# Optimization experiments

Measured on AMD Instinct MI355X. Metric: run time of the kernel, lower is better.

Reference implementation:

```python
import jax, jax.numpy as jnp
import numpy as np
import math

D = 512
H = 512


def setup_inputs() -> dict:
    key = jax.random.key(0)
    k1, k2, k3, k4 = jax.random.split(key, 4)
    x = jax.random.normal(k1, (32, 2048, D), dtype=jnp.float32)
    h0 = jax.random.normal(k2, (32, H), dtype=jnp.float32)
    Wx = jax.random.normal(k3, (D, 4 * H), dtype=jnp.float32) / math.sqrt(D)
    Wh = jax.random.normal(k4, (H, 4 * H), dtype=jnp.float32) / math.sqrt(H)
    b = jnp.zeros((4 * H,), dtype=jnp.float32)
    return {"x": x, "h0": h0, "Wx": Wx, "Wh": Wh, "b": b}


def lstm_forward(x, h0, Wx, Wh, b):
    # Precompute input projection for all timesteps: (N,T,4H)
    affine_x = jnp.einsum('ntd,dk->ntk', x, Wx) + b
    c0 = jnp.zeros_like(h0)
    Hdim = h0.shape[1]

    def step(carry, ax_t):
        h, c = carry
        affine = ax_t + h @ Wh  # (N,4H)
        i, f, o, g = jnp.split(affine, 4, axis=1)
        i = jax.nn.sigmoid(i)
        f = jax.nn.sigmoid(f)
        o = jax.nn.sigmoid(o)
        g = jnp.tanh(g)
        c_next = f * c + i * g
        h_next = o * jnp.tanh(c_next)
        return (h_next, c_next), h_next

    # scan over time: move T to leading axis
    (_, _), hs = jax.lax.scan(step, (h0, c0), jnp.swapaxes(affine_x, 0, 1))
    return jnp.swapaxes(hs, 0, 1)  # (N,T,H)


def reference(x, h0, Wx, Wh, b):
    return lstm_forward(x, h0, Wx, Wh, b)
```

## Files before the change

kernel.cpp:

```cpp
#include <hip/hip_runtime.h>

typedef __attribute__((ext_vector_type(8))) short short8;
typedef __attribute__((ext_vector_type(8))) unsigned short ushort8;
typedef __attribute__((ext_vector_type(4))) float f32x4;
typedef __attribute__((ext_vector_type(4))) int i32x4;

#define T_STEPS 2048

static __device__ __forceinline__ unsigned short f2bf(float f) {
  unsigned u = __builtin_bit_cast(unsigned, f);
  unsigned r = u + 0x7fffu + ((u >> 16) & 1u);
  return (unsigned short)(r >> 16);
}
static __device__ __forceinline__ float bf2f(unsigned short h) {
  unsigned u = ((unsigned)h) << 16;
  return __builtin_bit_cast(float, u);
}
static __device__ __forceinline__ float fast_sigmoid(float v) {
  return __builtin_amdgcn_rcpf(1.0f + __expf(-v));
}
static __device__ __forceinline__ float fast_tanh(float v) {
  return 1.0f - 2.0f * __builtin_amdgcn_rcpf(1.0f + __expf(2.0f * v));
}

__global__ void prep_kernel(const float* __restrict__ Wx, const float* __restrict__ Wh,
                            const float* __restrict__ h0,
                            unsigned short* __restrict__ wxp, unsigned short* __restrict__ whp,
                            unsigned short* __restrict__ hbuf, int* __restrict__ ctl,
                            int* __restrict__ flags) {
  int idx = blockIdx.x * 256 + threadIdx.x;
  if (idx < 2097152) {
    int which = idx >> 20;
    int r = idx & 1048575;
    int e = r & 7;
    int l = (r >> 3) & 63;
    int kt = (r >> 9) & 15;
    int g = (r >> 13) & 3;
    int s = r >> 15;
    int k = kt * 32 + ((l >> 4) << 3) + e;
    int c = g * 512 + s * 16 + (l & 15);
    const float* W = which ? Wh : Wx;
    unsigned short* dst = which ? whp : wxp;
    dst[r] = f2bf(W[k * 2048 + c]);
  } else if (idx < 2097152 + 16384) {
    int i = idx - 2097152;
    int bg = i >> 9;
    int k = i & 511;
    int g = bg >> 2, bl = bg & 3;
    float v = h0[i];
    unsigned short hi = f2bf(v) & 0xFFFCu;
    unsigned short lo = f2bf(v - bf2f(hi)) & 0xFFFCu;
    unsigned short* d = hbuf + g * 65536;
    d[bl * 512 + k] = hi;
    d[2048 + bl * 512 + k] = lo;
  } else if (idx < 2097152 + 16384 + 9) {
    ctl[idx - (2097152 + 16384)] = 0;
  } else if (idx < 2097152 + 16384 + 9 + 8192) {
    flags[idx - (2097152 + 16384 + 9)] = 0;
  }
}

__global__ void xprep_kernel(const float* __restrict__ x, unsigned short* __restrict__ xb) {
  size_t i8 = ((size_t)blockIdx.x * 256 + threadIdx.x) * 8;
  int t = (int)(i8 >> 14);
  int r = (int)(i8 & 16383);
  int b = r >> 9;
  int d = r & 511;
  const float* src = x + ((size_t)b * 2048 + (size_t)t) * 512 + d;
  f32x4 a = *(const f32x4*)src;
  f32x4 c = *(const f32x4*)(src + 4);
  ushort8 o;
#pragma unroll
  for (int e = 0; e < 4; ++e) {
    o[e] = f2bf(a[e]);
    o[e + 4] = f2bf(c[e]);
  }
  *(ushort8*)(xb + i8) = o;
}

__global__ __launch_bounds__(256, 1) void scan_kernel(
    const unsigned short* __restrict__ xb, const float* __restrict__ bias,
    const unsigned short* __restrict__ wxp, const unsigned short* __restrict__ whp,
    unsigned short* __restrict__ hbuf, float* __restrict__ out, int* __restrict__ ctl,
    int* __restrict__ flags) {
  __shared__ unsigned short WxL[4][16][512];
  __shared__ unsigned short WhL[4][16][512];
  __shared__ float gLDS[2][4][4][4][16];
  __shared__ int s_g, s_s, s_dir;

  const int tid = threadIdx.x;
  const int lane = tid & 63;
  const int gw = tid >> 6;

  if (tid == 0) {
    unsigned xcc;
    asm volatile("s_getreg_b32 %0, hwreg(HW_REG_XCC_ID)" : "=s"(xcc));
    xcc &= 7;
    int tk = __hip_atomic_fetch_add(&ctl[xcc], 1, __ATOMIC_RELAXED,
                                    __HIP_MEMORY_SCOPE_AGENT);
    int c[8];
    for (;;) {
      int tot = 0;
#pragma unroll
      for (int x = 0; x < 8; ++x) {
        c[x] = __hip_atomic_load(&ctl[x], __ATOMIC_RELAXED, __HIP_MEMORY_SCOPE_AGENT);
        tot += c[x];
      }
      if (tot >= 256) break;
      __builtin_amdgcn_s_sleep(2);
    }
    int g = -1, s = -1, dir = 0;
    if (tk < 32) {
      g = (int)xcc;
      s = tk;
      dir = (c[xcc] >= 32);
    } else {
      int rank = __hip_atomic_fetch_add(&ctl[8], 1, __ATOMIC_RELAXED,
                                        __HIP_MEMORY_SCOPE_AGENT);
      int acc2 = 0;
      for (int x = 0; x < 8; ++x) {
        int n = 32 - c[x];
        if (n < 0) n = 0;
        if (g < 0 && rank < acc2 + n) { g = x; s = c[x] + (rank - acc2); }
        acc2 += n;
      }
      dir = 0;
    }
    s_g = g; s_s = s; s_dir = dir;
  }
  __syncthreads();
  const int g = s_g, s = s_s, use_direct = s_dir;
  if (s < 0 || g < 0) return;

  {
    const ushort8* sx = (const ushort8*)(wxp + (size_t)s * 32768);
    const ushort8* sh = (const ushort8*)(whp + (size_t)s * 32768);
    ushort8* dx = (ushort8*)&WxL[0][0][0];
    ushort8* dh = (ushort8*)&WhL[0][0][0];
    for (int i = tid; i < 4096; i += 256) {
      dx[i] = sx[i];
      dh[i] = sh[i];
    }
  }
  __syncthreads();
  short8 wxf[4][4], whf[4][4];
#pragma unroll
  for (int kt = 0; kt < 4; ++kt)
#pragma unroll
    for (int nt = 0; nt < 4; ++nt) {
      const int ktg = (gw << 2) + kt;
      wxf[kt][nt] = *(const short8*)&WxL[nt][ktg][lane * 8];
      whf[kt][nt] = *(const short8*)&WhL[nt][ktg][lane * 8];
    }

  const int brow = lane & 3;
  const int kgrp = (lane >> 4) * 8;
  const int gb = lane >> 4;
  const int gu = lane & 15;
  float bias4[4];
#pragma unroll
  for (int gg2 = 0; gg2 < 4; ++gg2)
    bias4[gg2] = bias[gg2 * 512 + s * 16 + gu];
  float c = 0.f;

  unsigned short* hb = hbuf + g * 65536;
  int* gflags = flags + g * 1024;
  int* wflag = gflags + ((gw << 3) + (lane & 7)) * 32;
  int* myflag = gflags + s * 32;
  float* outbase = out + (size_t)(g * 4 + gb) * (2048 * 512) + s * 16 + gu;
  const int xrow = (g * 4 + brow) * 512;
  const int shfl_src = ((lane >> 3) << 4) + ((lane & 7) << 1);

  short8 xf[4];
#pragma unroll
  for (int kt = 0; kt < 4; ++kt) {
    const int k0 = (gw << 7) + (kt << 5) + kgrp;
    xf[kt] = *(const short8*)&xb[xrow + k0];
  }

  for (int t = 0; t < T_STEPS; ++t) {
    f32x4 acc[4], accl[4];
#pragma unroll
    for (int nt = 0; nt < 4; ++nt) {
      acc[nt] = (f32x4){0.f, 0.f, 0.f, 0.f};
      accl[nt] = (f32x4){0.f, 0.f, 0.f, 0.f};
    }
#pragma unroll
    for (int kt = 0; kt < 4; ++kt)
#pragma unroll
      for (int nt = 0; nt < 4; ++nt)
        acc[nt] = __builtin_amdgcn_mfma_f32_16x16x32_bf16(xf[kt], wxf[kt][nt], acc[nt], 0, 0, 0);

    const unsigned tag = (unsigned)((t >> 4) & 3);
    const unsigned tp32 = 0x00010001u * tag;
    const unsigned short* hrd = hb + (t & 15) * 4096;
    i32x4 q[8];
    bool ok = false;
    if (use_direct) {
#pragma unroll
      for (int kt = 0; kt < 4; ++kt) {
        const int k0 = (gw << 7) + (kt << 5) + kgrp;
        q[kt * 2 + 0] = *(const i32x4*)(hrd + brow * 512 + k0);
        q[kt * 2 + 1] = *(const i32x4*)(hrd + 2048 + brow * 512 + k0);
      }
      unsigned bad = 0;
#pragma unroll
      for (int i = 0; i < 8; ++i)
#pragma unroll
        for (int j = 0; j < 4; ++j)
          bad |= (((unsigned)q[i][j]) & 0x00030003u) ^ tp32;
      ok = __all(bad == 0);
    }

    if (!ok) {
      if (use_direct && t > 0) {
        int done = (lane >= 8);
        for (;;) {
          if (!done) {
            int old, zero = 0;
            asm volatile("global_atomic_add %0, %1, %2, off sc0\n\t"
                         "s_waitcnt vmcnt(0)"
                         : "=v"(old) : "v"(wflag), "v"(zero) : "memory");
            done = (old >= t);
          }
          if (__all(done)) break;
          __builtin_amdgcn_s_sleep(1);
        }
      }
      const unsigned long long tp64 = 0x0001000100010001ull * (unsigned long long)tag;
      const unsigned long long* h64 = (const unsigned long long*)hrd;
      for (;;) {
        unsigned long long bad = 0;
#pragma unroll
        for (int kt = 0; kt < 4; ++kt) {
          const int k0 = (gw << 7) + (kt << 5) + kgrp;
          const int bi = (brow * 512 + k0) >> 2;
          const int bj = (2048 + brow * 512 + k0) >> 2;
          union { unsigned long long u[2]; i32x4 v; } a, b;
          a.u[0] = __hip_atomic_load(h64 + bi, __ATOMIC_RELAXED, __HIP_MEMORY_SCOPE_AGENT);
          a.u[1] = __hip_atomic_load(h64 + bi + 1, __ATOMIC_RELAXED, __HIP_MEMORY_SCOPE_AGENT);
          b.u[0] = __hip_atomic_load(h64 + bj, __ATOMIC_RELAXED, __HIP_MEMORY_SCOPE_AGENT);
          b.u[1] = __hip_atomic_load(h64 + bj + 1, __ATOMIC_RELAXED, __HIP_MEMORY_SCOPE_AGENT);
          q[kt * 2 + 0] = a.v;
          q[kt * 2 + 1] = b.v;
          bad |= (a.u[0] & 0x0003000300030003ull) ^ tp64;
          bad |= (a.u[1] & 0x0003000300030003ull) ^ tp64;
          bad |= (b.u[0] & 0x0003000300030003ull) ^ tp64;
          bad |= (b.u[1] & 0x0003000300030003ull) ^ tp64;
        }
        if (__all(bad == 0)) break;
        __builtin_amdgcn_s_sleep(1);
      }
    }

#pragma unroll
    for (int kt = 0; kt < 4; ++kt) {
      short8 hh = __builtin_bit_cast(short8, q[kt * 2 + 0]);
      short8 hl = __builtin_bit_cast(short8, q[kt * 2 + 1]);
#pragma unroll
      for (int nt = 0; nt < 4; ++nt) {
        acc[nt] = __builtin_amdgcn_mfma_f32_16x16x32_bf16(hh, whf[kt][nt], acc[nt], 0, 0, 0);
        accl[nt] = __builtin_amdgcn_mfma_f32_16x16x32_bf16(hl, whf[kt][nt], accl[nt], 0, 0, 0);
      }
    }

    if (lane < 16) {
#pragma unroll
      for (int nt = 0; nt < 4; ++nt)
#pragma unroll
        for (int r = 0; r < 4; ++r)
          gLDS[t & 1][gw][nt][r][lane] = acc[nt][r] + accl[nt][r];
    }
    __syncthreads();

    float v4[4];
#pragma unroll
    for (int gg2 = 0; gg2 < 4; ++gg2) {
      float sum = bias4[gg2];
#pragma unroll
      for (int w = 0; w < 4; ++w) sum += gLDS[t & 1][w][gg2][gb][gu];
      v4[gg2] = sum;
    }
    float ig = fast_sigmoid(v4[0]);
    float fg = fast_sigmoid(v4[1]);
    float og = fast_sigmoid(v4[2]);
    float gg3 = fast_tanh(v4[3]);
    c = fg * c + ig * gg3;
    float h = og * fast_tanh(c);

    if (gw == 0 && t + 1 < T_STEPS) {
      const unsigned ntag = (unsigned)(((t + 1) >> 4) & 3);
      float ha = __shfl(h, shfl_src);
      float hbv = __shfl(h, shfl_src + 1);
      unsigned short hiA = (unsigned short)((f2bf(ha) & 0xFFFCu) | ntag);
      unsigned short loA = (unsigned short)((f2bf(ha - bf2f(hiA)) & 0xFFFCu) | ntag);
      unsigned short hiB = (unsigned short)((f2bf(hbv) & 0xFFFCu) | ntag);
      unsigned short loB = (unsigned short)((f2bf(hbv - bf2f(hiB)) & 0xFFFCu) | ntag);
      unsigned whi = (unsigned)hiA | ((unsigned)hiB << 16);
      unsigned wlo = (unsigned)loA | ((unsigned)loB << 16);
      if (lane < 32) {
        const int b = lane >> 3, u2 = (lane & 7) * 2;
        unsigned short* wr = hb + ((t + 1) & 15) * 4096;
        if (use_direct) {
          *(unsigned*)&wr[b * 512 + s * 16 + u2] = whi;
          *(unsigned*)&wr[2048 + b * 512 + s * 16 + u2] = wlo;
        } else {
          __hip_atomic_store((unsigned*)&wr[b * 512 + s * 16 + u2], whi,
                             __ATOMIC_RELAXED, __HIP_MEMORY_SCOPE_AGENT);
          __hip_atomic_store((unsigned*)&wr[2048 + b * 512 + s * 16 + u2], wlo,
                             __ATOMIC_RELAXED, __HIP_MEMORY_SCOPE_AGENT);
        }
      }
      asm volatile("s_waitcnt vmcnt(0)" ::: "memory");
      if (lane == 0) {
        int one = 1;
        asm volatile("global_atomic_add %0, %1, off" :: "v"(myflag), "v"(one) : "memory");
      }
    }

    if (gw == 1) outbase[(size_t)t * 512] = h;
    {
      const int tn = (t + 1 < T_STEPS) ? (t + 1) : t;
      const unsigned short* xt1 = xb + (size_t)tn * 16384;
#pragma unroll
      for (int kt = 0; kt < 4; ++kt) {
        const int k0 = (gw << 7) + (kt << 5) + kgrp;
        xf[kt] = *(const short8*)&xt1[xrow + k0];
      }
    }
  }
}

extern "C" void kernel_launch(void* const* d_in, const int* in_sizes, int n_in,
                              void* d_out, int out_size, void* d_ws, size_t ws_size,
                              hipStream_t stream) {
  const float* x = (const float*)d_in[0];
  const float* h0 = (const float*)d_in[1];
  const float* Wx = (const float*)d_in[2];
  const float* Wh = (const float*)d_in[3];
  const float* bias = (const float*)d_in[4];
  float* out = (float*)d_out;

  char* ws = (char*)d_ws;
  unsigned short* wxp = (unsigned short*)(ws);
  unsigned short* whp = (unsigned short*)(ws + (2u << 20));
  unsigned short* hbuf = (unsigned short*)(ws + (4u << 20));
  int* ctl = (int*)(ws + (5u << 20) + (512u << 10));
  int* flags = (int*)(ws + (6u << 20));
  unsigned short* xb = (unsigned short*)(ws + (8u << 20));

  hipLaunchKernelGGL(prep_kernel, dim3(8289), dim3(256), 0, stream,
                     Wx, Wh, h0, wxp, whp, hbuf, ctl, flags);
  hipLaunchKernelGGL(xprep_kernel, dim3(16384), dim3(256), 0, stream, x, xb);
  hipLaunchKernelGGL(scan_kernel, dim3(256), dim3(256), 0, stream,
                     xb, bias, wxp, whp, hbuf, out, ctl, flags);
}
```

Baseline: 6.269 ms.

## Replicate hidden-state broadcast buffers and issue h loads before the x MFMAs

Each step's h slot is now written in four replicated copies (ring depth 8 instead of 16, tag period changed to match). Readers poll alternate replicas, with a short sleep between tries, before falling back to the flag-based slow path. The h loads are also hoisted ahead of the input-projection MFMAs so their latency overlaps that compute. This aims to avoid stale cache lines and costly fallback polling in the cross-block spin-wait, at the cost of four times as many h stores per step and a larger workspace footprint, which moves the ctl and flags offsets.

```diff
diff --git a/kernel.cpp b/kernel.cpp
--- a/kernel.cpp
+++ b/kernel.cpp
@@ -50,9 +50,12 @@
     float v = h0[i];
     unsigned short hi = f2bf(v) & 0xFFFCu;
     unsigned short lo = f2bf(v - bf2f(hi)) & 0xFFFCu;
-    unsigned short* d = hbuf + g * 65536;
-    d[bl * 512 + k] = hi;
-    d[2048 + bl * 512 + k] = lo;
+    unsigned short* d = hbuf + g * 131072;
+#pragma unroll
+    for (int rep = 0; rep < 4; ++rep) {
+      d[rep * 4096 + bl * 512 + k] = hi;
+      d[rep * 4096 + 2048 + bl * 512 + k] = lo;
+    }
   } else if (idx < 2097152 + 16384 + 9) {
     ctl[idx - (2097152 + 16384)] = 0;
   } else if (idx < 2097152 + 16384 + 9 + 8192) {
@@ -163,7 +166,7 @@
     bias4[gg2] = bias[gg2 * 512 + s * 16 + gu];
   float c = 0.f;
 
-  unsigned short* hb = hbuf + g * 65536;
+  unsigned short* hb = hbuf + g * 131072;
   int* gflags = flags + g * 1024;
   int* wflag = gflags + ((gw << 3) + (lane & 7)) * 32;
   int* myflag = gflags + s * 32;
@@ -179,6 +182,21 @@
   }
 
   for (int t = 0; t < T_STEPS; ++t) {
+    const unsigned tag = (unsigned)((t >> 3) & 3);
+    const unsigned tp32 = 0x00010001u * tag;
+    const unsigned short* srd = hb + (t & 7) * 16384;
+    i32x4 q[8];
+    bool ok = false;
+
+    if (use_direct) {
+#pragma unroll
+      for (int kt = 0; kt < 4; ++kt) {
+        const int k0 = (gw << 7) + (kt << 5) + kgrp;
+        q[kt * 2 + 0] = *(const i32x4*)(srd + brow * 512 + k0);
+        q[kt * 2 + 1] = *(const i32x4*)(srd + 2048 + brow * 512 + k0);
+      }
+    }
+
     f32x4 acc[4], accl[4];
 #pragma unroll
     for (int nt = 0; nt < 4; ++nt) {
@@ -191,18 +209,7 @@
       for (int nt = 0; nt < 4; ++nt)
         acc[nt] = __builtin_amdgcn_mfma_f32_16x16x32_bf16(xf[kt], wxf[kt][nt], acc[nt], 0, 0, 0);
 
-    const unsigned tag = (unsigned)((t >> 4) & 3);
-    const unsigned tp32 = 0x00010001u * tag;
-    const unsigned short* hrd = hb + (t & 15) * 4096;
-    i32x4 q[8];
-    bool ok = false;
     if (use_direct) {
-#pragma unroll
-      for (int kt = 0; kt < 4; ++kt) {
-        const int k0 = (gw << 7) + (kt << 5) + kgrp;
-        q[kt * 2 + 0] = *(const i32x4*)(hrd + brow * 512 + k0);
-        q[kt * 2 + 1] = *(const i32x4*)(hrd + 2048 + brow * 512 + k0);
-      }
       unsigned bad = 0;
 #pragma unroll
       for (int i = 0; i < 8; ++i)
@@ -210,6 +217,23 @@
         for (int j = 0; j < 4; ++j)
           bad |= (((unsigned)q[i][j]) & 0x00030003u) ^ tp32;
       ok = __all(bad == 0);
+      for (int rep = 1; rep < 4 && !ok; ++rep) {
+        __builtin_amdgcn_s_sleep(2);
+        const unsigned short* hrd = srd + rep * 4096;
+#pragma unroll
+        for (int kt = 0; kt < 4; ++kt) {
+          const int k0 = (gw << 7) + (kt << 5) + kgrp;
+          q[kt * 2 + 0] = *(const i32x4*)(hrd + brow * 512 + k0);
+          q[kt * 2 + 1] = *(const i32x4*)(hrd + 2048 + brow * 512 + k0);
+        }
+        unsigned bad2 = 0;
+#pragma unroll
+        for (int i = 0; i < 8; ++i)
+#pragma unroll
+          for (int j = 0; j < 4; ++j)
+            bad2 |= (((unsigned)q[i][j]) & 0x00030003u) ^ tp32;
+        ok = __all(bad2 == 0);
+      }
     }
 
     if (!ok) {
@@ -228,7 +252,7 @@
         }
       }
       const unsigned long long tp64 = 0x0001000100010001ull * (unsigned long long)tag;
-      const unsigned long long* h64 = (const unsigned long long*)hrd;
+      const unsigned long long* h64 = (const unsigned long long*)srd;
       for (;;) {
         unsigned long long bad = 0;
 #pragma unroll
@@ -289,7 +313,7 @@
     float h = og * fast_tanh(c);
 
     if (gw == 0 && t + 1 < T_STEPS) {
-      const unsigned ntag = (unsigned)(((t + 1) >> 4) & 3);
+      const unsigned ntag = (unsigned)(((t + 1) >> 3) & 3);
       float ha = __shfl(h, shfl_src);
       float hbv = __shfl(h, shfl_src + 1);
       unsigned short hiA = (unsigned short)((f2bf(ha) & 0xFFFCu) | ntag);
@@ -300,15 +324,21 @@
       unsigned wlo = (unsigned)loA | ((unsigned)loB << 16);
       if (lane < 32) {
         const int b = lane >> 3, u2 = (lane & 7) * 2;
-        unsigned short* wr = hb + ((t + 1) & 15) * 4096;
+        unsigned short* wr = hb + ((t + 1) & 7) * 16384;
         if (use_direct) {
-          *(unsigned*)&wr[b * 512 + s * 16 + u2] = whi;
-          *(unsigned*)&wr[2048 + b * 512 + s * 16 + u2] = wlo;
+#pragma unroll
+          for (int rep = 0; rep < 4; ++rep) {
+            *(unsigned*)&wr[rep * 4096 + b * 512 + s * 16 + u2] = whi;
+            *(unsigned*)&wr[rep * 4096 + 2048 + b * 512 + s * 16 + u2] = wlo;
+          }
         } else {
-          __hip_atomic_store((unsigned*)&wr[b * 512 + s * 16 + u2], whi,
-                             __ATOMIC_RELAXED, __HIP_MEMORY_SCOPE_AGENT);
-          __hip_atomic_store((unsigned*)&wr[2048 + b * 512 + s * 16 + u2], wlo,
-                             __ATOMIC_RELAXED, __HIP_MEMORY_SCOPE_AGENT);
+#pragma unroll
+          for (int rep = 0; rep < 4; ++rep) {
+            __hip_atomic_store((unsigned*)&wr[rep * 4096 + b * 512 + s * 16 + u2], whi,
+                               __ATOMIC_RELAXED, __HIP_MEMORY_SCOPE_AGENT);
+            __hip_atomic_store((unsigned*)&wr[rep * 4096 + 2048 + b * 512 + s * 16 + u2], wlo,
+                               __ATOMIC_RELAXED, __HIP_MEMORY_SCOPE_AGENT);
+          }
         }
       }
       asm volatile("s_waitcnt vmcnt(0)" ::: "memory");
@@ -345,8 +375,8 @@
   unsigned short* wxp = (unsigned short*)(ws);
   unsigned short* whp = (unsigned short*)(ws + (2u << 20));
   unsigned short* hbuf = (unsigned short*)(ws + (4u << 20));
-  int* ctl = (int*)(ws + (5u << 20) + (512u << 10));
-  int* flags = (int*)(ws + (6u << 20));
+  int* ctl = (int*)(ws + (6u << 20) + (512u << 10));
+  int* flags = (int*)(ws + (7u << 20));
   unsigned short* xb = (unsigned short*)(ws + (8u << 20));
 
   hipLaunchKernelGGL(prep_kernel, dim3(8289), dim3(256), 0, stream,
```

New measurement: 6.583 ms. 1.05x slower.
